# Kernel optimization log

Measured on AMD Instinct MI355X. Metric: run time of the kernel, lower is better.

## Reference

```python
import jax, jax.numpy as jnp
import numpy as np

DIM = 768
D_INNER = 2 * DIM
D_STATE = 16
D_CONV = 4
DT_RANK = (DIM + 15) // 16  # 48
B, L = 8, 2048


def _mamba_params(key, tag):
    ks = jax.random.split(key, 8)
    s = lambda k, shape, fan: jax.random.normal(k, shape, jnp.float32) * (fan ** -0.5)
    p = {}
    p[tag + '_in_w'] = s(ks[0], (2 * D_INNER, DIM), DIM)
    p[tag + '_conv_w'] = s(ks[1], (D_INNER, 1, D_CONV), D_CONV)
    p[tag + '_conv_b'] = jnp.zeros((D_INNER,), jnp.float32)
    p[tag + '_xproj_w'] = s(ks[2], (DT_RANK + 2 * D_STATE, D_INNER), D_INNER)
    p[tag + '_dt_w'] = s(ks[3], (D_INNER, DT_RANK), DT_RANK)
    p[tag + '_dt_b'] = jax.random.uniform(ks[4], (D_INNER,), jnp.float32, -4.0, -2.0)  # ~log(dt) init
    # S4D-real init: A = -(1..d_state)
    p[tag + '_A_log'] = jnp.log(jnp.broadcast_to(jnp.arange(1, D_STATE + 1, dtype=jnp.float32), (D_INNER, D_STATE)))
    p[tag + '_D'] = jnp.ones((D_INNER,), jnp.float32)
    p[tag + '_out_w'] = s(ks[5], (DIM, D_INNER), D_INNER)
    return p


def setup_inputs() -> dict:
    key = jax.random.key(0)
    k1, k2, k3, k4, k5 = jax.random.split(key, 5)
    inp = {
        'hidden_states': jax.random.normal(k1, (B, L, DIM), jnp.float32),
        'residual': jax.random.normal(k2, (B, L, DIM), jnp.float32),
        'norm_w': jnp.ones((DIM,), jnp.float32),
        'norm_b': jnp.zeros((DIM,), jnp.float32),
        'lin_w': jax.random.normal(k5, (DIM, DIM), jnp.float32) * (DIM ** -0.5),
        'lin_b': jnp.zeros((DIM,), jnp.float32),
    }
    inp.update(_mamba_params(k3, 'f'))
    inp.update(_mamba_params(k4, 'r'))
    return inp


def _layernorm(x, w, b, eps=1e-5):
    mu = jnp.mean(x, axis=-1, keepdims=True)
    var = jnp.var(x, axis=-1, keepdims=True)
    return (x - mu) * jax.lax.rsqrt(var + eps) * w + b


def _mamba(x, in_w, conv_w, conv_b, xproj_w, dt_w, dt_b, A_log, Dp, out_w):
    b, l, _ = x.shape
    # input projection -> x branch and gate z
    xz = jnp.einsum('bld,ed->ble', x, in_w)  # (B,L,2*d_inner)
    xc, z = jnp.split(xz, 2, axis=-1)
    # causal depthwise conv over time
    xt = jnp.transpose(xc, (0, 2, 1))  # (B, d_inner, L)
    xt = jax.lax.conv_general_dilated(
        xt, conv_w, window_strides=(1,), padding=[(D_CONV - 1, 0)],
        dimension_numbers=('NCH', 'OIH', 'NCH'), feature_group_count=D_INNER)
    xt = xt + conv_b[None, :, None]
    u = jax.nn.silu(jnp.transpose(xt, (0, 2, 1)))  # (B,L,d_inner)
    # input-dependent SSM params
    x_dbl = jnp.einsum('bld,ed->ble', u, xproj_w)
    dt, Bm, Cm = jnp.split(x_dbl, [DT_RANK, DT_RANK + D_STATE], axis=-1)
    delta = jax.nn.softplus(jnp.einsum('blr,dr->bld', dt, dt_w) + dt_b)
    A = -jnp.exp(A_log)  # (d_inner, d_state)

    def step(h, inp):
        d_t, b_t, c_t, u_t = inp  # (B,d_inner) (B,d_state) (B,d_state) (B,d_inner)
        dA = jnp.exp(d_t[..., None] * A)  # (B,d_inner,d_state)
        h = dA * h + (d_t * u_t)[..., None] * b_t[:, None, :]
        y = jnp.einsum('bds,bs->bd', h, c_t)
        return h, y

    h0 = jnp.zeros((b, D_INNER, D_STATE), x.dtype)
    xs = (jnp.swapaxes(delta, 0, 1), jnp.swapaxes(Bm, 0, 1),
          jnp.swapaxes(Cm, 0, 1), jnp.swapaxes(u, 0, 1))
    _, ys = jax.lax.scan(step, h0, xs)
    y = jnp.swapaxes(ys, 0, 1) + u * Dp
    y = y * jax.nn.silu(z)
    return jnp.einsum('ble,de->bld', y, out_w)


def reference(hidden_states, residual, norm_w, norm_b,
              f_in_w, f_conv_w, f_conv_b, f_xproj_w, f_dt_w, f_dt_b, f_A_log, f_D, f_out_w,
              r_in_w, r_conv_w, r_conv_b, r_xproj_w, r_dt_w, r_dt_b, r_A_log, r_D, r_out_w,
              lin_w, lin_b):
    res = hidden_states + residual
    h_norm = _layernorm(res, norm_w, norm_b)
    h = _mamba(h_norm, f_in_w, f_conv_w, f_conv_b, f_xproj_w, f_dt_w, f_dt_b, f_A_log, f_D, f_out_w)
    h_inv = _mamba(jnp.flip(h_norm, axis=-2), r_in_w, r_conv_w, r_conv_b, r_xproj_w, r_dt_w, r_dt_b, r_A_log, r_D, r_out_w)
    h = h + jnp.flip(h_inv, axis=-2)
    h = jnp.einsum('bld,ed->ble', h, lin_w) + lin_b
    return (h, res)
```

## Files before the change

### kernel.cpp

```cpp
#include <hip/hip_runtime.h>
#include <stdint.h>
#include <stddef.h>

#define DIMX   768
#define DINNER 1536
#define DSTATE 16
#define DTRANK 48
#define BB     8
#define LL     2048
#define MM     (BB*LL)
#define NC     16
#define CLEN   (LL/NC)

typedef float f32x4 __attribute__((ext_vector_type(4)));
typedef __bf16 bf16x8 __attribute__((ext_vector_type(8)));
struct us4 { unsigned short x, y, z, w; };

__device__ __forceinline__ float b2f(unsigned short u) {
  union { unsigned int i; float f; } v; v.i = ((unsigned int)u) << 16; return v.f;
}
__device__ __forceinline__ unsigned short f2b(float f) {
  union { float f; unsigned int i; } v; v.f = f;
  unsigned int r = v.i + 0x7FFFu + ((v.i >> 16) & 1u);
  return (unsigned short)(r >> 16);
}
__device__ __forceinline__ float sigf(float x){ return 1.f/(1.f+__expf(-x)); }
__device__ __forceinline__ float softplusf(float x){ return fmaxf(x,0.f) + log1pf(__expf(-fabsf(x))); }

__device__ __forceinline__ void async16(const unsigned short* g, unsigned short* l) {
  __builtin_amdgcn_global_load_lds(
      (__attribute__((address_space(1))) void*)(g),
      (__attribute__((address_space(3))) void*)(l), 16, 0, 0);
}

__global__ void __launch_bounds__(256)
cvt_k(const float* __restrict__ s, unsigned short* __restrict__ d, int n4)
{
  const int i = blockIdx.x * 256 + threadIdx.x;
  if (i < n4) {
    const float4 v = ((const float4*)s)[i];
    us4 o; o.x = f2b(v.x); o.y = f2b(v.y); o.z = f2b(v.z); o.w = f2b(v.w);
    ((us4*)d)[i] = o;
  }
}

template<int EPI>
__global__ void __launch_bounds__(256)
gemm_bt(const unsigned short* __restrict__ A,
        const unsigned short* __restrict__ Bw,
        void* __restrict__ C0, void* __restrict__ C1,
        const float* __restrict__ bias,
        int N, int K)
{
  __shared__ __align__(16) unsigned short As[128*64];
  __shared__ __align__(16) unsigned short Bs[128*64];
  const int tid  = threadIdx.x;
  const int wave = tid >> 6, lane = tid & 63;
  const int bm = blockIdx.x, bn = blockIdx.y;
  const int wm = wave & 1, wn = wave >> 1;
  const int r16 = lane & 15, quad = lane >> 4;

  f32x4 acc[4][4] = {};

  const unsigned short* Ab = A  + (size_t)bm * 128 * K;
  const unsigned short* Bb = Bw + (size_t)bn * 128 * K;
  const int e0 = wave * 2048 + lane * 8;

  for (int kt = 0; kt < K; kt += 64) {
#pragma unroll
    for (int i = 0; i < 4; ++i) {
      const int e   = e0 + i * 512;
      const int row = e >> 6;
      const int col = e & 63;
      async16(Ab + (size_t)row * K + kt + col, &As[e]);
      async16(Bb + (size_t)row * K + kt + col, &Bs[e]);
    }
    __syncthreads();
#pragma unroll
    for (int ks = 0; ks < 2; ++ks) {
      bf16x8 af[4], bfr[4];
#pragma unroll
      for (int mt = 0; mt < 4; ++mt)
        af[mt] = *(const bf16x8*)&As[(wm*64 + mt*16 + r16)*64 + ks*32 + quad*8];
#pragma unroll
      for (int nt = 0; nt < 4; ++nt)
        bfr[nt] = *(const bf16x8*)&Bs[(wn*64 + nt*16 + r16)*64 + ks*32 + quad*8];
#pragma unroll
      for (int mt = 0; mt < 4; ++mt)
#pragma unroll
        for (int nt = 0; nt < 4; ++nt)
          acc[mt][nt] = __builtin_amdgcn_mfma_f32_16x16x32_bf16(af[mt], bfr[nt], acc[mt][nt], 0, 0, 0);
    }
    __syncthreads();
  }

#pragma unroll
  for (int nt = 0; nt < 4; ++nt) {
    const int col = bn*128 + wn*64 + nt*16 + r16;
    float bv = 0.f;
    if (EPI == 2 || EPI == 3) bv = bias[col];
#pragma unroll
    for (int mt = 0; mt < 4; ++mt) {
#pragma unroll
      for (int rg = 0; rg < 4; ++rg) {
        const size_t row = (size_t)bm*128 + wm*64 + mt*16 + quad*4 + rg;
        const float v = acc[mt][nt][rg];
        if (EPI == 0)      ((unsigned short*)C0)[row*(size_t)N + col] = f2b(v);
        else if (EPI == 1) ((float*)C0)[row*(size_t)N + col] = v;
        else if (EPI == 2) ((unsigned short*)C0)[row*(size_t)N + col] = f2b(softplusf(v + bv));
        else if (EPI == 3) ((float*)C0)[row*(size_t)N + col] = v + bv;
        else {
          if (col < 1536) ((unsigned short*)C0)[row*1536 + col] = f2b(v);
          else            ((unsigned short*)C1)[row*1536 + (col - 1536)] = f2b(v);
        }
      }
    }
  }
}

__global__ void __launch_bounds__(256)
add_ln_k(const float* __restrict__ hs, const float* __restrict__ rsd,
         const float* __restrict__ nw, const float* __restrict__ nb,
         float* __restrict__ res_out,
         unsigned short* __restrict__ hn_f, unsigned short* __restrict__ hn_r)
{
  const int wave = threadIdx.x >> 6, lane = threadIdx.x & 63;
  const int row = blockIdx.x * 4 + wave;
  const int b = row >> 11, l = row & 2047;
  const size_t off = (size_t)row * DIMX;
  float4 x[3];
  float s1 = 0.f, s2 = 0.f;
#pragma unroll
  for (int i = 0; i < 3; ++i) {
    const int c = lane*4 + i*256;
    const float4 a = *(const float4*)&hs[off + c];
    const float4 r = *(const float4*)&rsd[off + c];
    float4 v; v.x = a.x + r.x; v.y = a.y + r.y; v.z = a.z + r.z; v.w = a.w + r.w;
    x[i] = v;
    *(float4*)&res_out[off + c] = v;
    s1 += v.x + v.y + v.z + v.w;
    s2 += v.x*v.x + v.y*v.y + v.z*v.z + v.w*v.w;
  }
#pragma unroll
  for (int s = 32; s >= 1; s >>= 1) { s1 += __shfl_xor(s1, s); s2 += __shfl_xor(s2, s); }
  const float mu = s1 * (1.f/768.f);
  const float var = s2 * (1.f/768.f) - mu*mu;
  const float rstd = rsqrtf(var + 1e-5f);
  const size_t roff = (((size_t)b << 11) + (2047 - l)) * DIMX;
#pragma unroll
  for (int i = 0; i < 3; ++i) {
    const int c = lane*4 + i*256;
    us4 o;
    o.x = f2b((x[i].x - mu)*rstd*nw[c+0] + nb[c+0]);
    o.y = f2b((x[i].y - mu)*rstd*nw[c+1] + nb[c+1]);
    o.z = f2b((x[i].z - mu)*rstd*nw[c+2] + nb[c+2]);
    o.w = f2b((x[i].w - mu)*rstd*nw[c+3] + nb[c+3]);
    *(us4*)&hn_f[off + c]  = o;
    *(us4*)&hn_r[roff + c] = o;
  }
}

__global__ void __launch_bounds__(256)
conv_silu_k(const unsigned short* __restrict__ xc,
            const float* __restrict__ cw,
            const float* __restrict__ cb,
            unsigned short* __restrict__ u)
{
  const int d  = blockIdx.x * 256 + threadIdx.x;
  const int l0 = blockIdx.y * 8;
  const size_t b = blockIdx.z;
  const float4 w = *(const float4*)&cw[d*4];
  const float bias = cb[d];
  float x[11];
#pragma unroll
  for (int i = 0; i < 11; ++i) {
    const int l = l0 - 3 + i;
    x[i] = (l >= 0) ? b2f(xc[((size_t)b*LL + l)*DINNER + d]) : 0.f;
  }
#pragma unroll
  for (int i = 0; i < 8; ++i) {
    const float acc = bias + w.x*x[i] + w.y*x[i+1] + w.z*x[i+2] + w.w*x[i+3];
    u[((size_t)b*LL + l0 + i)*DINNER + d] = f2b(acc * sigf(acc));
  }
}

__global__ void __launch_bounds__(256)
prep_pads_k(const float* __restrict__ fx, const float* __restrict__ rx,
            const float* __restrict__ fdw, const float* __restrict__ rdw,
            unsigned short* __restrict__ fxp, unsigned short* __restrict__ rxp,
            unsigned short* __restrict__ fdwp, unsigned short* __restrict__ rdwp)
{
  const int idx = blockIdx.x * 256 + threadIdx.x;
  if (idx < 128*1536) {
    const int n = idx / 1536, k = idx - n*1536;
    fxp[idx] = (n < 80) ? f2b(fx[n*1536 + k]) : (unsigned short)0;
    rxp[idx] = (n < 80) ? f2b(rx[n*1536 + k]) : (unsigned short)0;
  }
  if (idx < 1536*64) {
    const int n = idx >> 6, k = idx & 63;
    fdwp[idx] = (k < 48) ? f2b(fdw[n*48 + k]) : (unsigned short)0;
    rdwp[idx] = (k < 48) ? f2b(rdw[n*48 + k]) : (unsigned short)0;
  }
}

__global__ void __launch_bounds__(256)
split_dt_k(const float* __restrict__ xdbl, unsigned short* __restrict__ dtp)
{
  const int idx = blockIdx.x * 256 + threadIdx.x;
  const int row = idx >> 6, c = idx & 63;
  const float v = (c < 48) ? xdbl[(size_t)row*128 + c] : 0.f;
  dtp[idx] = f2b(v);
}

__global__ void __launch_bounds__(256)
scan_part1_k(const unsigned short* __restrict__ delta,
             const unsigned short* __restrict__ u,
             const float* __restrict__ xdbl,
             const float* __restrict__ A_log,
             float* __restrict__ S, float* __restrict__ sdel)
{
  const int d = blockIdx.x * 256 + threadIdx.x;
  const int c = blockIdx.y;
  const size_t b = blockIdx.z;
  const float A1 = -__expf(A_log[d*DSTATE]);

  const size_t r0 = b*LL + (size_t)c*CLEN;
  const unsigned short* dp = delta + r0*DINNER + d;
  const unsigned short* up = u     + r0*DINNER + d;
  const float* bp = xdbl + r0*128 + 48;

  float h[16];
#pragma unroll
  for (int s = 0; s < 16; ++s) h[s] = 0.f;
  float sd = 0.f;

  float del = b2f(*dp), uu = b2f(*up);
  f32x4 Bv[4];
#pragma unroll
  for (int i = 0; i < 4; ++i) Bv[i] = ((const f32x4*)bp)[i];

  for (int t = 0; t < CLEN; ++t) {
    const float del_c = del, uu_c = uu;
    f32x4 Bc[4];
#pragma unroll
    for (int i = 0; i < 4; ++i) Bc[i] = Bv[i];
    if (t + 1 < CLEN) {
      dp += DINNER; up += DINNER; bp += 128;
      del = b2f(*dp); uu = b2f(*up);
#pragma unroll
      for (int i = 0; i < 4; ++i) Bv[i] = ((const f32x4*)bp)[i];
    }
    sd += del_c;
    const float e1 = __expf(del_c * A1);
    const float du = del_c * uu_c;
    float a = e1;
#pragma unroll
    for (int i = 0; i < 4; ++i)
#pragma unroll
      for (int j = 0; j < 4; ++j) {
        const int s = i*4 + j;
        h[s] = a*h[s] + du*Bc[i][j];
        if (s < 15) a *= e1;
      }
  }
  float* Sp = S + ((b*NC + c)*(size_t)DINNER + d)*16;
#pragma unroll
  for (int i = 0; i < 4; ++i) {
    f32x4 v; v[0]=h[i*4]; v[1]=h[i*4+1]; v[2]=h[i*4+2]; v[3]=h[i*4+3];
    ((f32x4*)Sp)[i] = v;
  }
  sdel[(b*NC + c)*DINNER + d] = sd;
}

__global__ void __launch_bounds__(256)
scan_comb_k(float* __restrict__ S, const float* __restrict__ sdel,
            const float* __restrict__ A_log)
{
  const int idx = blockIdx.x * 256 + threadIdx.x;
  const int sg = idx & 3;
  const int x  = idx >> 2;
  const int b  = x / DINNER;
  const int d  = x - b*DINNER;

  float Aj[4];
#pragma unroll
  for (int j = 0; j < 4; ++j) Aj[j] = -__expf(A_log[d*DSTATE + sg*4 + j]);

  f32x4 h; h.x=0.f; h.y=0.f; h.z=0.f; h.w=0.f;
  for (int c = 0; c < NC; ++c) {
    const size_t si = (((size_t)b*NC + c)*DINNER + d)*16 + sg*4;
    const f32x4 Sc = *(const f32x4*)&S[si];
    const float sd = sdel[((size_t)b*NC + c)*DINNER + d];
    *(f32x4*)&S[si] = h;
    f32x4 nh;
    nh.x = Sc.x + __expf(Aj[0]*sd)*h.x;
    nh.y = Sc.y + __expf(Aj[1]*sd)*h.y;
    nh.z = Sc.z + __expf(Aj[2]*sd)*h.z;
    nh.w = Sc.w + __expf(Aj[3]*sd)*h.w;
    h = nh;
  }
}

__global__ void __launch_bounds__(256)
scan_part2_k(const unsigned short* __restrict__ delta,
             const unsigned short* __restrict__ u,
             const unsigned short* __restrict__ z,
             const float* __restrict__ xdbl,
             const float* __restrict__ A_log,
             const float* __restrict__ Dp,
             const float* __restrict__ S,
             unsigned short* __restrict__ yg)
{
  const int d = blockIdx.x * 256 + threadIdx.x;
  const int c = blockIdx.y;
  const size_t b = blockIdx.z;
  const float A1 = -__expf(A_log[d*DSTATE]);
  const float Dv = Dp[d];

  float h[16];
  const float* Sp = S + ((b*NC + c)*(size_t)DINNER + d)*16;
#pragma unroll
  for (int i = 0; i < 4; ++i) {
    const f32x4 v = ((const f32x4*)Sp)[i];
    h[i*4]=v[0]; h[i*4+1]=v[1]; h[i*4+2]=v[2]; h[i*4+3]=v[3];
  }

  const size_t r0 = b*LL + (size_t)c*CLEN;
  const unsigned short* dp = delta + r0*DINNER + d;
  const unsigned short* up = u     + r0*DINNER + d;
  const unsigned short* zp = z     + r0*DINNER + d;
  const float* bp = xdbl + r0*128 + 48;
  unsigned short* yp = yg + r0*DINNER + d;

  float del = b2f(*dp), uu = b2f(*up), zz = b2f(*zp);
  f32x4 Bv[4], Cv[4];
#pragma unroll
  for (int i = 0; i < 4; ++i) { Bv[i] = ((const f32x4*)bp)[i]; Cv[i] = ((const f32x4*)bp)[i+4]; }

  for (int t = 0; t < CLEN; ++t) {
    const float del_c = del, uu_c = uu, zz_c = zz;
    f32x4 Bc[4], Cc[4];
#pragma unroll
    for (int i = 0; i < 4; ++i) { Bc[i] = Bv[i]; Cc[i] = Cv[i]; }
    if (t + 1 < CLEN) {
      dp += DINNER; up += DINNER; zp += DINNER; bp += 128;
      del = b2f(*dp); uu = b2f(*up); zz = b2f(*zp);
#pragma unroll
      for (int i = 0; i < 4; ++i) { Bv[i] = ((const f32x4*)bp)[i]; Cv[i] = ((const f32x4*)bp)[i+4]; }
    }
    const float e1 = __expf(del_c * A1);
    const float du = del_c * uu_c;
    float a = e1;
    float y0 = 0.f, y1 = 0.f;
#pragma unroll
    for (int i = 0; i < 4; ++i)
#pragma unroll
      for (int j = 0; j < 4; ++j) {
        const int s = i*4 + j;
        h[s] = a*h[s] + du*Bc[i][j];
        if (i < 2) y0 += h[s]*Cc[i][j]; else y1 += h[s]*Cc[i][j];
        if (s < 15) a *= e1;
      }
    const float yD = y0 + y1 + uu_c * Dv;
    *yp = f2b(yD * zz_c * sigf(zz_c));
    yp += DINNER;
  }
}

__global__ void __launch_bounds__(256)
combine_k(const unsigned short* __restrict__ of, const unsigned short* __restrict__ orv,
          unsigned short* __restrict__ hsum)
{
  const int idx = blockIdx.x * 256 + threadIdx.x;
  const int row = idx / 768, c = idx - row*768;
  const int b = row >> 11, l = row & 2047;
  const size_t rrow = ((size_t)b << 11) + (2047 - l);
  hsum[idx] = f2b(b2f(of[idx]) + b2f(orv[rrow*768 + c]));
}

extern "C" void kernel_launch(void* const* d_in, const int* in_sizes, int n_in,
                              void* d_out, int out_size, void* d_ws, size_t ws_size,
                              hipStream_t stream)
{
  (void)in_sizes; (void)n_in; (void)out_size;
  const float* hs   = (const float*)d_in[0];
  const float* rsd  = (const float*)d_in[1];
  const float* nw   = (const float*)d_in[2];
  const float* nb   = (const float*)d_in[3];
  const float* linw = (const float*)d_in[4];
  const float* linb = (const float*)d_in[5];
  const float* inw[2] = {(const float*)d_in[6],  (const float*)d_in[15]};
  const float* cvw[2] = {(const float*)d_in[7],  (const float*)d_in[16]};
  const float* cvb[2] = {(const float*)d_in[8],  (const float*)d_in[17]};
  const float* xpw[2] = {(const float*)d_in[9],  (const float*)d_in[18]};
  const float* dtw[2] = {(const float*)d_in[10], (const float*)d_in[19]};
  const float* dtb[2] = {(const float*)d_in[11], (const float*)d_in[20]};
  const float* alg[2] = {(const float*)d_in[12], (const float*)d_in[21]};
  const float* ddp[2] = {(const float*)d_in[13], (const float*)d_in[22]};
  const float* otw[2] = {(const float*)d_in[14], (const float*)d_in[23]};

  float* out_h   = (float*)d_out;
  float* out_res = out_h + (size_t)MM * DIMX;

  char* base = (char*)d_ws; size_t off = 0;
  auto alloc = [&](size_t bytes) -> void* {
    void* p = base + off; off = (off + bytes + 255) & ~(size_t)255; return p;
  };

  const size_t SZ_HN   = (size_t)MM * DIMX   * 2;
  const size_t SZ_1536 = (size_t)MM * DINNER * 2;
  const size_t SZ_XDBL = (size_t)MM * 128 * 4;
  const size_t SZ_DTP  = (size_t)MM * 64 * 2;
  const size_t SZ_XPP  = (size_t)128 * 1536 * 2;
  const size_t SZ_DWP  = (size_t)1536 * 64 * 2;
  const size_t SZ_INW  = (size_t)3072 * 768 * 2;
  const size_t SZ_OTW  = (size_t)768 * 1536 * 2;
  const size_t SZ_LNW  = (size_t)768 * 768 * 2;
  const size_t SZ_S    = (size_t)BB * NC * DINNER * 16 * 4;
  const size_t SZ_SD   = (size_t)BB * NC * DINNER * 4;

  unsigned short *hn[2], *xcb[2], *zb[2], *ub[2], *dl[2], *dtp[2], *outb[2], *hsum;
  float* xdb[2];
  float *scanS[2], *scanSd[2];
  unsigned short *xpp[2], *dwp[2], *inwb[2], *otwb[2], *linwb;

  const bool conc = ws_size >= (size_t)640000000;

  if (conc) {
    hn[0] = (unsigned short*)alloc(SZ_HN);
    hn[1] = (unsigned short*)alloc(SZ_HN);
    for (int i = 0; i < 2; ++i) {
      xcb[i]  = (unsigned short*)alloc(SZ_1536);
      zb[i]   = (unsigned short*)alloc(SZ_1536);
      ub[i]   = (unsigned short*)alloc(SZ_1536);
      dl[i]   = (unsigned short*)alloc(SZ_1536);
      xdb[i]  = (float*)alloc(SZ_XDBL);
      dtp[i]  = (unsigned short*)alloc(SZ_DTP);
      outb[i] = (unsigned short*)alloc(SZ_HN);
      scanS[i]  = (float*)alloc(SZ_S);
      scanSd[i] = (float*)alloc(SZ_SD);
    }
    hsum = (unsigned short*)alloc(SZ_HN);
  } else {
    hn[0] = (unsigned short*)alloc(SZ_HN);
    hn[1] = (unsigned short*)alloc(SZ_HN);
    unsigned short* xc_s  = (unsigned short*)alloc(SZ_1536);
    unsigned short* z_s   = (unsigned short*)alloc(SZ_1536);
    unsigned short* u_s   = (unsigned short*)alloc(SZ_1536);
    unsigned short* dl_s  = (unsigned short*)alloc(SZ_1536);
    float*          xd_s  = (float*)alloc(SZ_XDBL);
    unsigned short* dtp_s = (unsigned short*)alloc(SZ_DTP);
    for (int i = 0; i < 2; ++i) {
      xcb[i]=xc_s; zb[i]=z_s; ub[i]=u_s; dl[i]=dl_s; xdb[i]=xd_s; dtp[i]=dtp_s;
      scanS[i]  = (float*)((char*)hn[i]);
      scanSd[i] = (float*)((char*)hn[i] + SZ_S);
    }
    outb[0] = hn[0];
    outb[1] = xc_s;
    hsum    = u_s;
  }
  for (int i = 0; i < 2; ++i) {
    xpp[i]  = (unsigned short*)alloc(SZ_XPP);
    dwp[i]  = (unsigned short*)alloc(SZ_DWP);
    inwb[i] = (unsigned short*)alloc(SZ_INW);
    otwb[i] = (unsigned short*)alloc(SZ_OTW);
  }
  linwb = (unsigned short*)alloc(SZ_LNW);

  auto cvt = [&](const float* s, unsigned short* d, int n) {
    cvt_k<<<(n/4 + 255)/256, 256, 0, stream>>>(s, d, n/4);
  };
  for (int i = 0; i < 2; ++i) {
    cvt(inw[i], inwb[i], 3072*768);
    cvt(otw[i], otwb[i], 768*1536);
  }
  cvt(linw, linwb, 768*768);
  prep_pads_k<<<768, 256, 0, stream>>>(xpw[0], xpw[1], dtw[0], dtw[1],
                                       xpp[0], xpp[1], dwp[0], dwp[1]);
  add_ln_k<<<4096, 256, 0, stream>>>(hs, rsd, nw, nb, out_res, hn[0], hn[1]);

  auto pre_dir = [&](int i) {
    gemm_bt<4><<<dim3(MM/128, 3072/128), 256, 0, stream>>>(hn[i], inwb[i], xcb[i], zb[i], nullptr, 3072, 768);
    conv_silu_k<<<dim3(DINNER/256, LL/8, BB), 256, 0, stream>>>(xcb[i], cvw[i], cvb[i], ub[i]);
    gemm_bt<1><<<dim3(MM/128, 1), 256, 0, stream>>>(ub[i], xpp[i], xdb[i], nullptr, nullptr, 128, 1536);
    split_dt_k<<<(MM*64)/256, 256, 0, stream>>>(xdb[i], dtp[i]);
    gemm_bt<2><<<dim3(MM/128, 1536/128), 256, 0, stream>>>(dtp[i], dwp[i], dl[i], nullptr, dtb[i], 1536, 64);
  };
  auto scan_dir = [&](int i) {
    scan_part1_k<<<dim3(DINNER/256, NC, BB), 256, 0, stream>>>(dl[i], ub[i], xdb[i], alg[i], scanS[i], scanSd[i]);
    scan_comb_k<<<192, 256, 0, stream>>>(scanS[i], scanSd[i], alg[i]);
    scan_part2_k<<<dim3(DINNER/256, NC, BB), 256, 0, stream>>>(dl[i], ub[i], zb[i], xdb[i], alg[i], ddp[i], scanS[i], ub[i]);
  };
  auto post_dir = [&](int i) {
    gemm_bt<0><<<dim3(MM/128, 768/128), 256, 0, stream>>>(ub[i], otwb[i], outb[i], nullptr, nullptr, 768, 1536);
  };

  pre_dir(0); scan_dir(0); post_dir(0);
  pre_dir(1); scan_dir(1); post_dir(1);

  combine_k<<<(MM*DIMX)/256, 256, 0, stream>>>(outb[0], outb[1], hsum);
  gemm_bt<3><<<dim3(MM/128, 768/128), 256, 0, stream>>>(hsum, linwb, out_h, nullptr, linb, 768, 768);
}
```

Measured before the change: 1.337 ms.

## Fold out_proj into final linear, flip rows in GEMM loads, swizzle LDS

Precomputes per-direction effective weights lin_w·out_w with a small GEMM, so each direction's scan output projects straight to the final output. The old out-projection GEMMs, the combine kernel and the final linear GEMM go away; the reverse direction accumulates into the output through a row-flipped epilogue. The reverse-direction input is no longer materialised: the in-projection GEMM reads hn with row index XOR 2047. LDS tiles also get an XOR swizzle to reduce bank conflicts. The costs are two 1536-K output GEMMs where there were 768/1536-K pairs, an fp32 read-modify-write of the output, and bf16 rounding of the fused weights, which could affect accuracy.

```diff
diff --git a/kernel.cpp b/kernel.cpp
--- a/kernel.cpp
+++ b/kernel.cpp
@@ -44,7 +44,15 @@
   }
 }
 
-template<int EPI>
+__global__ void __launch_bounds__(256)
+tr_k(const float* __restrict__ w, unsigned short* __restrict__ wt)
+{
+  const int idx = blockIdx.x * 256 + threadIdx.x;
+  const int e = idx / 768, d = idx - e*768;
+  wt[idx] = f2b(w[d*1536 + e]);
+}
+
+template<int EPI, int AFLIP>
 __global__ void __launch_bounds__(256)
 gemm_bt(const unsigned short* __restrict__ A,
         const unsigned short* __restrict__ Bw,
@@ -62,29 +70,38 @@
 
   f32x4 acc[4][4] = {};
 
-  const unsigned short* Ab = A  + (size_t)bm * 128 * K;
   const unsigned short* Bb = Bw + (size_t)bn * 128 * K;
   const int e0 = wave * 2048 + lane * 8;
 
   for (int kt = 0; kt < K; kt += 64) {
 #pragma unroll
     for (int i = 0; i < 4; ++i) {
-      const int e   = e0 + i * 512;
-      const int row = e >> 6;
-      const int col = e & 63;
-      async16(Ab + (size_t)row * K + kt + col, &As[e]);
-      async16(Bb + (size_t)row * K + kt + col, &Bs[e]);
+      const int e  = e0 + i * 512;
+      const int r  = e >> 6;
+      const int cs = (e & 63) >> 3;
+      const int cg = cs ^ (r & 7);
+      const int col = cg * 8;
+      int garow = bm*128 + r;
+      if (AFLIP) garow ^= 2047;
+      async16(A  + (size_t)garow * K + kt + col, &As[e]);
+      async16(Bb + (size_t)r * K + kt + col, &Bs[e]);
     }
     __syncthreads();
 #pragma unroll
     for (int ks = 0; ks < 2; ++ks) {
       bf16x8 af[4], bfr[4];
 #pragma unroll
-      for (int mt = 0; mt < 4; ++mt)
-        af[mt] = *(const bf16x8*)&As[(wm*64 + mt*16 + r16)*64 + ks*32 + quad*8];
-#pragma unroll
-      for (int nt = 0; nt < 4; ++nt)
-        bfr[nt] = *(const bf16x8*)&Bs[(wn*64 + nt*16 + r16)*64 + ks*32 + quad*8];
+      for (int mt = 0; mt < 4; ++mt) {
+        const int R = wm*64 + mt*16 + r16;
+        const int c = (ks*4 + quad) ^ (R & 7);
+        af[mt] = *(const bf16x8*)&As[R*64 + c*8];
+      }
+#pragma unroll
+      for (int nt = 0; nt < 4; ++nt) {
+        const int R = wn*64 + nt*16 + r16;
+        const int c = (ks*4 + quad) ^ (R & 7);
+        bfr[nt] = *(const bf16x8*)&Bs[R*64 + c*8];
+      }
 #pragma unroll
       for (int mt = 0; mt < 4; ++mt)
 #pragma unroll
@@ -103,13 +120,17 @@
     for (int mt = 0; mt < 4; ++mt) {
 #pragma unroll
       for (int rg = 0; rg < 4; ++rg) {
-        const size_t row = (size_t)bm*128 + wm*64 + mt*16 + quad*4 + rg;
+        const int irow = bm*128 + wm*64 + mt*16 + quad*4 + rg;
+        const size_t row = (size_t)irow;
         const float v = acc[mt][nt][rg];
         if (EPI == 0)      ((unsigned short*)C0)[row*(size_t)N + col] = f2b(v);
         else if (EPI == 1) ((float*)C0)[row*(size_t)N + col] = v;
         else if (EPI == 2) ((unsigned short*)C0)[row*(size_t)N + col] = f2b(softplusf(v + bv));
         else if (EPI == 3) ((float*)C0)[row*(size_t)N + col] = v + bv;
-        else {
+        else if (EPI == 6) {
+          float* p = (float*)C0 + (size_t)(irow ^ 2047)*N + col;
+          *p += v;
+        } else {
           if (col < 1536) ((unsigned short*)C0)[row*1536 + col] = f2b(v);
           else            ((unsigned short*)C1)[row*1536 + (col - 1536)] = f2b(v);
         }
@@ -121,12 +142,10 @@
 __global__ void __launch_bounds__(256)
 add_ln_k(const float* __restrict__ hs, const float* __restrict__ rsd,
          const float* __restrict__ nw, const float* __restrict__ nb,
-         float* __restrict__ res_out,
-         unsigned short* __restrict__ hn_f, unsigned short* __restrict__ hn_r)
+         float* __restrict__ res_out, unsigned short* __restrict__ hn)
 {
   const int wave = threadIdx.x >> 6, lane = threadIdx.x & 63;
   const int row = blockIdx.x * 4 + wave;
-  const int b = row >> 11, l = row & 2047;
   const size_t off = (size_t)row * DIMX;
   float4 x[3];
   float s1 = 0.f, s2 = 0.f;
@@ -146,7 +165,6 @@
   const float mu = s1 * (1.f/768.f);
   const float var = s2 * (1.f/768.f) - mu*mu;
   const float rstd = rsqrtf(var + 1e-5f);
-  const size_t roff = (((size_t)b << 11) + (2047 - l)) * DIMX;
 #pragma unroll
   for (int i = 0; i < 3; ++i) {
     const int c = lane*4 + i*256;
@@ -155,8 +173,7 @@
     o.y = f2b((x[i].y - mu)*rstd*nw[c+1] + nb[c+1]);
     o.z = f2b((x[i].z - mu)*rstd*nw[c+2] + nb[c+2]);
     o.w = f2b((x[i].w - mu)*rstd*nw[c+3] + nb[c+3]);
-    *(us4*)&hn_f[off + c]  = o;
-    *(us4*)&hn_r[roff + c] = o;
+    *(us4*)&hn[off + c] = o;
   }
 }
 
@@ -367,22 +384,11 @@
   }
 }
 
-__global__ void __launch_bounds__(256)
-combine_k(const unsigned short* __restrict__ of, const unsigned short* __restrict__ orv,
-          unsigned short* __restrict__ hsum)
-{
-  const int idx = blockIdx.x * 256 + threadIdx.x;
-  const int row = idx / 768, c = idx - row*768;
-  const int b = row >> 11, l = row & 2047;
-  const size_t rrow = ((size_t)b << 11) + (2047 - l);
-  hsum[idx] = f2b(b2f(of[idx]) + b2f(orv[rrow*768 + c]));
-}
-
 extern "C" void kernel_launch(void* const* d_in, const int* in_sizes, int n_in,
                               void* d_out, int out_size, void* d_ws, size_t ws_size,
                               hipStream_t stream)
 {
-  (void)in_sizes; (void)n_in; (void)out_size;
+  (void)in_sizes; (void)n_in; (void)out_size; (void)ws_size;
   const float* hs   = (const float*)d_in[0];
   const float* rsd  = (const float*)d_in[1];
   const float* nw   = (const float*)d_in[2];
@@ -414,90 +420,63 @@
   const size_t SZ_XPP  = (size_t)128 * 1536 * 2;
   const size_t SZ_DWP  = (size_t)1536 * 64 * 2;
   const size_t SZ_INW  = (size_t)3072 * 768 * 2;
-  const size_t SZ_OTW  = (size_t)768 * 1536 * 2;
+  const size_t SZ_WT   = (size_t)1536 * 768 * 2;
   const size_t SZ_LNW  = (size_t)768 * 768 * 2;
   const size_t SZ_S    = (size_t)BB * NC * DINNER * 16 * 4;
   const size_t SZ_SD   = (size_t)BB * NC * DINNER * 4;
 
-  unsigned short *hn[2], *xcb[2], *zb[2], *ub[2], *dl[2], *dtp[2], *outb[2], *hsum;
-  float* xdb[2];
-  float *scanS[2], *scanSd[2];
-  unsigned short *xpp[2], *dwp[2], *inwb[2], *otwb[2], *linwb;
-
-  const bool conc = ws_size >= (size_t)640000000;
-
-  if (conc) {
-    hn[0] = (unsigned short*)alloc(SZ_HN);
-    hn[1] = (unsigned short*)alloc(SZ_HN);
-    for (int i = 0; i < 2; ++i) {
-      xcb[i]  = (unsigned short*)alloc(SZ_1536);
-      zb[i]   = (unsigned short*)alloc(SZ_1536);
-      ub[i]   = (unsigned short*)alloc(SZ_1536);
-      dl[i]   = (unsigned short*)alloc(SZ_1536);
-      xdb[i]  = (float*)alloc(SZ_XDBL);
-      dtp[i]  = (unsigned short*)alloc(SZ_DTP);
-      outb[i] = (unsigned short*)alloc(SZ_HN);
-      scanS[i]  = (float*)alloc(SZ_S);
-      scanSd[i] = (float*)alloc(SZ_SD);
-    }
-    hsum = (unsigned short*)alloc(SZ_HN);
-  } else {
-    hn[0] = (unsigned short*)alloc(SZ_HN);
-    hn[1] = (unsigned short*)alloc(SZ_HN);
-    unsigned short* xc_s  = (unsigned short*)alloc(SZ_1536);
-    unsigned short* z_s   = (unsigned short*)alloc(SZ_1536);
-    unsigned short* u_s   = (unsigned short*)alloc(SZ_1536);
-    unsigned short* dl_s  = (unsigned short*)alloc(SZ_1536);
-    float*          xd_s  = (float*)alloc(SZ_XDBL);
-    unsigned short* dtp_s = (unsigned short*)alloc(SZ_DTP);
-    for (int i = 0; i < 2; ++i) {
-      xcb[i]=xc_s; zb[i]=z_s; ub[i]=u_s; dl[i]=dl_s; xdb[i]=xd_s; dtp[i]=dtp_s;
-      scanS[i]  = (float*)((char*)hn[i]);
-      scanSd[i] = (float*)((char*)hn[i] + SZ_S);
-    }
-    outb[0] = hn[0];
-    outb[1] = xc_s;
-    hsum    = u_s;
-  }
+  unsigned short* hn   = (unsigned short*)alloc(SZ_HN);
+  unsigned short* xc_s = (unsigned short*)alloc(SZ_1536);
+  unsigned short* z_s  = (unsigned short*)alloc(SZ_1536);
+  unsigned short* u_s  = (unsigned short*)alloc(SZ_1536);
+  unsigned short* dl_s = (unsigned short*)alloc(SZ_1536);
+  float*          xd_s = (float*)alloc(SZ_XDBL);
+  unsigned short* dtp_s= (unsigned short*)alloc(SZ_DTP);
+  float*          scanS  = (float*)alloc(SZ_S);
+  float*          scanSd = (float*)alloc(SZ_SD);
+  unsigned short *xpp[2], *dwp[2], *inwb[2], *wtb[2], *weff[2];
   for (int i = 0; i < 2; ++i) {
     xpp[i]  = (unsigned short*)alloc(SZ_XPP);
     dwp[i]  = (unsigned short*)alloc(SZ_DWP);
     inwb[i] = (unsigned short*)alloc(SZ_INW);
-    otwb[i] = (unsigned short*)alloc(SZ_OTW);
-  }
-  linwb = (unsigned short*)alloc(SZ_LNW);
+    wtb[i]  = (unsigned short*)alloc(SZ_WT);
+    weff[i] = (unsigned short*)alloc(SZ_WT);
+  }
+  unsigned short* linwb = (unsigned short*)alloc(SZ_LNW);
 
   auto cvt = [&](const float* s, unsigned short* d, int n) {
     cvt_k<<<(n/4 + 255)/256, 256, 0, stream>>>(s, d, n/4);
   };
   for (int i = 0; i < 2; ++i) {
     cvt(inw[i], inwb[i], 3072*768);
-    cvt(otw[i], otwb[i], 768*1536);
+    tr_k<<<(1536*768)/256, 256, 0, stream>>>(otw[i], wtb[i]);
   }
   cvt(linw, linwb, 768*768);
   prep_pads_k<<<768, 256, 0, stream>>>(xpw[0], xpw[1], dtw[0], dtw[1],
                                        xpp[0], xpp[1], dwp[0], dwp[1]);
-  add_ln_k<<<4096, 256, 0, stream>>>(hs, rsd, nw, nb, out_res, hn[0], hn[1]);
+  for (int i = 0; i < 2; ++i)
+    gemm_bt<0,0><<<dim3(6, 12), 256, 0, stream>>>(linwb, wtb[i], weff[i], nullptr, nullptr, 1536, 768);
+
+  add_ln_k<<<4096, 256, 0, stream>>>(hs, rsd, nw, nb, out_res, hn);
 
   auto pre_dir = [&](int i) {
-    gemm_bt<4><<<dim3(MM/128, 3072/128), 256, 0, stream>>>(hn[i], inwb[i], xcb[i], zb[i], nullptr, 3072, 768);
-    conv_silu_k<<<dim3(DINNER/256, LL/8, BB), 256, 0, stream>>>(xcb[i], cvw[i], cvb[i], ub[i]);
-    gemm_bt<1><<<dim3(MM/128, 1), 256, 0, stream>>>(ub[i], xpp[i], xdb[i], nullptr, nullptr, 128, 1536);
-    split_dt_k<<<(MM*64)/256, 256, 0, stream>>>(xdb[i], dtp[i]);
-    gemm_bt<2><<<dim3(MM/128, 1536/128), 256, 0, stream>>>(dtp[i], dwp[i], dl[i], nullptr, dtb[i], 1536, 64);
+    if (i == 0)
+      gemm_bt<4,0><<<dim3(MM/128, 3072/128), 256, 0, stream>>>(hn, inwb[0], xc_s, z_s, nullptr, 3072, 768);
+    else
+      gemm_bt<4,1><<<dim3(MM/128, 3072/128), 256, 0, stream>>>(hn, inwb[1], xc_s, z_s, nullptr, 3072, 768);
+    conv_silu_k<<<dim3(DINNER/256, LL/8, BB), 256, 0, stream>>>(xc_s, cvw[i], cvb[i], u_s);
+    gemm_bt<1,0><<<dim3(MM/128, 1), 256, 0, stream>>>(u_s, xpp[i], xd_s, nullptr, nullptr, 128, 1536);
+    split_dt_k<<<(MM*64)/256, 256, 0, stream>>>(xd_s, dtp_s);
+    gemm_bt<2,0><<<dim3(MM/128, 1536/128), 256, 0, stream>>>(dtp_s, dwp[i], dl_s, nullptr, dtb[i], 1536, 64);
   };
   auto scan_dir = [&](int i) {
-    scan_part1_k<<<dim3(DINNER/256, NC, BB), 256, 0, stream>>>(dl[i], ub[i], xdb[i], alg[i], scanS[i], scanSd[i]);
-    scan_comb_k<<<192, 256, 0, stream>>>(scanS[i], scanSd[i], alg[i]);
-    scan_part2_k<<<dim3(DINNER/256, NC, BB), 256, 0, stream>>>(dl[i], ub[i], zb[i], xdb[i], alg[i], ddp[i], scanS[i], ub[i]);
+    scan_part1_k<<<dim3(DINNER/256, NC, BB), 256, 0, stream>>>(dl_s, u_s, xd_s, alg[i], scanS, scanSd);
+    scan_comb_k<<<192, 256, 0, stream>>>(scanS, scanSd, alg[i]);
+    scan_part2_k<<<dim3(DINNER/256, NC, BB), 256, 0, stream>>>(dl_s, u_s, z_s, xd_s, alg[i], ddp[i], scanS, u_s);
   };
-  auto post_dir = [&](int i) {
-    gemm_bt<0><<<dim3(MM/128, 768/128), 256, 0, stream>>>(ub[i], otwb[i], outb[i], nullptr, nullptr, 768, 1536);
-  };
-
-  pre_dir(0); scan_dir(0); post_dir(0);
-  pre_dir(1); scan_dir(1); post_dir(1);
-
-  combine_k<<<(MM*DIMX)/256, 256, 0, stream>>>(outb[0], outb[1], hsum);
-  gemm_bt<3><<<dim3(MM/128, 768/128), 256, 0, stream>>>(hsum, linwb, out_h, nullptr, linb, 768, 768);
-}
+
+  pre_dir(0); scan_dir(0);
+  gemm_bt<3,0><<<dim3(MM/128, 768/128), 256, 0, stream>>>(u_s, weff[0], out_h, nullptr, linb, 768, 1536);
+  pre_dir(1); scan_dir(1);
+  gemm_bt<6,0><<<dim3(MM/128, 768/128), 256, 0, stream>>>(u_s, weff[1], out_h, nullptr, nullptr, 768, 1536);
+}
```

New measurement: 1.268 ms. 1.05x faster.
